# Optimization experiments

Hardware: AMD Instinct MI355X
Metric: run time of the kernel (lower is better)

Reference implementation:

```python
import jax, jax.numpy as jnp
import numpy as np

N_NODES = 10000
N_EDGES = 25000
D_FEAT = 128

def setup_inputs() -> dict:
    key = jax.random.key(0)
    k1, k2, k3 = jax.random.split(key, 3)
    x = jax.random.normal(k1, (N_NODES, D_FEAT), dtype=jnp.float32)
    edge_attr = jax.random.normal(k2, (N_EDGES, D_FEAT), dtype=jnp.float32)
    edge_index = jax.random.randint(k3, (2, N_EDGES), 0, N_NODES, dtype=jnp.int64)
    return {"x": x, "edge_attr": edge_attr, "edge_index": edge_index}

def reference(x, edge_attr, edge_index):
    # lg_node_idx: [E, 2] (src, dst) pairs; each original edge becomes a line-graph node
    lg_node_idx = edge_index.T
    # gather endpoint features and average -> [E, d]
    new_x = x[lg_node_idx].mean(axis=1)
    # stack([x, edge_attr], dim=2).mean(dim=2) == elementwise average
    new_x = (new_x + edge_attr) * 0.5
    col0 = lg_node_idx[:, 0]  # src of each edge
    col1 = lg_node_idx[:, 1]  # dst of each edge
    # edge i -> edge j connected iff dst(i) == src(j) and src(i) != dst(j)
    mask = (col1[:, None] == col0[None, :]) & (col0[:, None] != col1[None, :])  # [E, E]
    rows, cols = jnp.nonzero(mask)  # data-dependent size; eager (non-jit) reference
    lg_edge_index = jnp.stack([rows, cols], axis=0)  # [2, E_lg]
    # attr of line-graph edge = feature of shared node's incoming edge's dst entry
    lg_edge_attr_idx = lg_node_idx[rows][:, 1]
    lg_edge_attr = new_x[lg_edge_attr_idx]
    return new_x, lg_edge_index, lg_edge_attr
```

## Files before the change

### kernel.cpp

```cpp
#include <hip/hip_runtime.h>

#define NN 10000
#define NE 25000
#define DF 128
#define SB 256
#define NBLK ((NE + SB - 1) / SB)
#define NEWXB ((NE * 32 + SB - 1) / SB)

__global__ void k_init(int* __restrict__ head, int* __restrict__ gFlag) {
    int tid = blockIdx.x * blockDim.x + threadIdx.x;
    if (tid < NN) head[tid] = -1;
    if (tid < NBLK) gFlag[tid] = 0;
}

__global__ void k_link(const int* __restrict__ c0,
                       int* __restrict__ head, int* __restrict__ nxt) {
    int j = blockIdx.x * blockDim.x + threadIdx.x;
    if (j >= NE) return;
    nxt[j] = atomicExch(&head[c0[j]], j);
}

__global__ __launch_bounds__(SB) void k_scan_newx(const float* __restrict__ x,
                                                  const float* __restrict__ ea,
                                                  const int* __restrict__ c0,
                                                  const int* __restrict__ c1,
                                                  const int* __restrict__ head,
                                                  const int* __restrict__ nxt,
                                                  int* __restrict__ gFlag,
                                                  int* __restrict__ rowStart,
                                                  float* __restrict__ out) {
    int b = blockIdx.x, t = threadIdx.x;

    if (b >= NBLK) {
        int tid = (b - NBLK) * SB + t;
        if (tid >= NE * 32) return;
        int e = tid >> 5, q = tid & 31;
        int u = c0[e], v = c1[e];
        float4 a  = ((const float4*)(x + (size_t)u * DF))[q];
        float4 bb = ((const float4*)(x + (size_t)v * DF))[q];
        float4 c  = ((const float4*)(ea + (size_t)e * DF))[q];
        float4 r;
        r.x = ((a.x + bb.x) * 0.5f + c.x) * 0.5f;
        r.y = ((a.y + bb.y) * 0.5f + c.y) * 0.5f;
        r.z = ((a.z + bb.z) * 0.5f + c.z) * 0.5f;
        r.w = ((a.w + bb.w) * 0.5f + c.w) * 0.5f;
        ((float4*)(out + (size_t)e * DF))[q] = r;
        return;
    }

    __shared__ int sc[SB];
    __shared__ int sr[SB];
    int i = b * SB + t;
    int cnt = 0;
    if (i < NE) {
        int u = c0[i], v = c1[i];
        for (int j = head[v]; j != -1; j = nxt[j])
            if (c1[j] != u) ++cnt;
    }
    sc[t] = cnt;
    __syncthreads();
    for (int off = 1; off < SB; off <<= 1) {
        int add = (t >= off) ? sc[t - off] : 0;
        __syncthreads();
        sc[t] += add;
        __syncthreads();
    }
    int blockSum = sc[SB - 1];
    if (t == 0) atomicExch(&gFlag[b], blockSum + 1);
    int val = 0;
    if (t < b) {
        int v2;
        do { v2 = atomicAdd(&gFlag[t], 0); } while (v2 == 0);
        val = v2 - 1;
    }
    sr[t] = val;
    __syncthreads();
    for (int off = SB / 2; off > 0; off >>= 1) {
        if (t < off) sr[t] += sr[t + off];
        __syncthreads();
    }
    int base = sr[0];
    if (i < NE) rowStart[i] = base + sc[t] - cnt;
    if (b == NBLK - 1 && t == 0) rowStart[NE] = base + blockSum;
}

__global__ void k_emit(const float* __restrict__ newx,
                       const int* __restrict__ c0, const int* __restrict__ c1,
                       const int* __restrict__ head, const int* __restrict__ nxt,
                       const int* __restrict__ rowStart,
                       float* __restrict__ outRows, float* __restrict__ outCols,
                       float* __restrict__ outAttr) {
    int gtid = blockIdx.x * blockDim.x + threadIdx.x;
    int i = gtid >> 6, lane = gtid & 63;
    if (i >= NE) return;
    int base = rowStart[i];
    int cnt  = rowStart[i + 1] - base;
    if (cnt == 0) return;
    int u = c0[i], v = c1[i];

    int myj = -1, B = 0;
    for (int j = head[v]; j != -1; j = nxt[j], ++B)
        if (B == lane) myj = j;

    if (B <= 64) {
        int myc1 = (myj >= 0) ? c1[myj] : -1;
        bool keep = (myj >= 0) && (myc1 != u);
        int rank = 0;
        for (int q = 0; q < B; ++q) {
            int jq = __shfl(myj, q);
            int cq = __shfl(myc1, q);
            if (cq != u && jq < myj) ++rank;
        }
        if (keep) {
            outRows[base + rank] = (float)i;
            outCols[base + rank] = (float)myj;
        }
    } else {
        int pos = 0;
        for (int j = head[v]; j != -1; j = nxt[j], ++pos) {
            if ((pos & 63) != lane) continue;
            if (c1[j] == u) continue;
            int rank = 0;
            for (int j2 = head[v]; j2 != -1; j2 = nxt[j2])
                rank += (c1[j2] != u && j2 < j) ? 1 : 0;
            outRows[base + rank] = (float)i;
            outCols[base + rank] = (float)j;
        }
    }

    float4 val = ((const float4*)(newx + (size_t)v * DF))[lane & 31];
    for (int tt = (lane >> 5); tt < cnt; tt += 2)
        ((float4*)(outAttr + (size_t)(base + tt) * DF))[lane & 31] = val;
}


extern "C" void kernel_launch(void* const* d_in, const int* in_sizes, int n_in,
                              void* d_out, int out_size, void* d_ws, size_t ws_size,
                              hipStream_t stream) {
    const float* x  = (const float*)d_in[0];
    const float* ea = (const float*)d_in[1];
    const int*   ei = (const int*)d_in[2];
    const int* c0 = ei;
    const int* c1 = ei + NE;

    float* out = (float*)d_out;
    int E_lg = (out_size - NE * DF) / (DF + 2);
    if (E_lg < 0) E_lg = 0;

    float* out_newx = out;
    float* out_rows = out + (size_t)NE * DF;
    float* out_cols = out_rows + E_lg;
    float* out_attr = out_cols + E_lg;

    int* ws       = (int*)d_ws;
    int* head     = ws;
    int* nxt      = head + NN;
    int* rowStart = nxt + NE;
    int* gFlag    = rowStart + NE + 1;

    k_init<<<(NN + SB - 1) / SB, SB, 0, stream>>>(head, gFlag);
    k_link<<<(NE + SB - 1) / SB, SB, 0, stream>>>(c0, head, nxt);
    k_scan_newx<<<NBLK + NEWXB, SB, 0, stream>>>(x, ea, c0, c1, head, nxt,
                                                 gFlag, rowStart, out_newx);
    k_emit<<<(NE * 64 + SB - 1) / SB, SB, 0, stream>>>(out_newx, c0, c1, head, nxt,
                                                       rowStart, out_rows, out_cols, out_attr);
}
```

Baseline: 40.34 us.

## Move newx into init kernel and emit indices inside scan kernel

Measured after the change: 47.15 us. 1.17x slower.

```diff
diff --git a/kernel.cpp b/kernel.cpp
--- a/kernel.cpp
+++ b/kernel.cpp
@@ -7,10 +7,27 @@
 #define NBLK ((NE + SB - 1) / SB)
 #define NEWXB ((NE * 32 + SB - 1) / SB)
 
-__global__ void k_init(int* __restrict__ head, int* __restrict__ gFlag) {
+typedef float f4 __attribute__((ext_vector_type(4)));
+
+__global__ void k_newx_init(const float* __restrict__ x, const float* __restrict__ ea,
+                            const int* __restrict__ c0, const int* __restrict__ c1,
+                            float* __restrict__ out, int* __restrict__ head,
+                            int* __restrict__ gFlag) {
     int tid = blockIdx.x * blockDim.x + threadIdx.x;
     if (tid < NN) head[tid] = -1;
     if (tid < NBLK) gFlag[tid] = 0;
+    if (tid >= NE * 32) return;
+    int e = tid >> 5, q = tid & 31;
+    int u = c0[e], v = c1[e];
+    float4 a  = ((const float4*)(x + (size_t)u * DF))[q];
+    float4 bb = ((const float4*)(x + (size_t)v * DF))[q];
+    float4 c  = ((const float4*)(ea + (size_t)e * DF))[q];
+    float4 r;
+    r.x = ((a.x + bb.x) * 0.5f + c.x) * 0.5f;
+    r.y = ((a.y + bb.y) * 0.5f + c.y) * 0.5f;
+    r.z = ((a.z + bb.z) * 0.5f + c.z) * 0.5f;
+    r.w = ((a.w + bb.w) * 0.5f + c.w) * 0.5f;
+    ((float4*)(out + (size_t)e * DF))[q] = r;
 }
 
 __global__ void k_link(const int* __restrict__ c0,
@@ -20,40 +37,21 @@
     nxt[j] = atomicExch(&head[c0[j]], j);
 }
 
-__global__ __launch_bounds__(SB) void k_scan_newx(const float* __restrict__ x,
-                                                  const float* __restrict__ ea,
-                                                  const int* __restrict__ c0,
-                                                  const int* __restrict__ c1,
-                                                  const int* __restrict__ head,
-                                                  const int* __restrict__ nxt,
-                                                  int* __restrict__ gFlag,
-                                                  int* __restrict__ rowStart,
-                                                  float* __restrict__ out) {
-    int b = blockIdx.x, t = threadIdx.x;
-
-    if (b >= NBLK) {
-        int tid = (b - NBLK) * SB + t;
-        if (tid >= NE * 32) return;
-        int e = tid >> 5, q = tid & 31;
-        int u = c0[e], v = c1[e];
-        float4 a  = ((const float4*)(x + (size_t)u * DF))[q];
-        float4 bb = ((const float4*)(x + (size_t)v * DF))[q];
-        float4 c  = ((const float4*)(ea + (size_t)e * DF))[q];
-        float4 r;
-        r.x = ((a.x + bb.x) * 0.5f + c.x) * 0.5f;
-        r.y = ((a.y + bb.y) * 0.5f + c.y) * 0.5f;
-        r.z = ((a.z + bb.z) * 0.5f + c.z) * 0.5f;
-        r.w = ((a.w + bb.w) * 0.5f + c.w) * 0.5f;
-        ((float4*)(out + (size_t)e * DF))[q] = r;
-        return;
-    }
-
+__global__ __launch_bounds__(SB) void k_scan_idx(const int* __restrict__ c0,
+                                                 const int* __restrict__ c1,
+                                                 const int* __restrict__ head,
+                                                 const int* __restrict__ nxt,
+                                                 int* __restrict__ gFlag,
+                                                 float* __restrict__ outRows,
+                                                 float* __restrict__ outCols,
+                                                 int* __restrict__ attrSrc) {
     __shared__ int sc[SB];
     __shared__ int sr[SB];
+    int b = blockIdx.x, t = threadIdx.x;
     int i = b * SB + t;
-    int cnt = 0;
+    int u = 0, v = 0, cnt = 0;
     if (i < NE) {
-        int u = c0[i], v = c1[i];
+        u = c0[i]; v = c1[i];
         for (int j = head[v]; j != -1; j = nxt[j])
             if (c1[j] != u) ++cnt;
     }
@@ -79,58 +77,35 @@
         if (t < off) sr[t] += sr[t + off];
         __syncthreads();
     }
-    int base = sr[0];
-    if (i < NE) rowStart[i] = base + sc[t] - cnt;
-    if (b == NBLK - 1 && t == 0) rowStart[NE] = base + blockSum;
-}
+    int base = sr[0] + sc[t] - cnt;
 
-__global__ void k_emit(const float* __restrict__ newx,
-                       const int* __restrict__ c0, const int* __restrict__ c1,
-                       const int* __restrict__ head, const int* __restrict__ nxt,
-                       const int* __restrict__ rowStart,
-                       float* __restrict__ outRows, float* __restrict__ outCols,
-                       float* __restrict__ outAttr) {
-    int gtid = blockIdx.x * blockDim.x + threadIdx.x;
-    int i = gtid >> 6, lane = gtid & 63;
-    if (i >= NE) return;
-    int base = rowStart[i];
-    int cnt  = rowStart[i + 1] - base;
-    if (cnt == 0) return;
-    int u = c0[i], v = c1[i];
-
-    int myj = -1, B = 0;
-    for (int j = head[v]; j != -1; j = nxt[j], ++B)
-        if (B == lane) myj = j;
-
-    if (B <= 64) {
-        int myc1 = (myj >= 0) ? c1[myj] : -1;
-        bool keep = (myj >= 0) && (myc1 != u);
-        int rank = 0;
-        for (int q = 0; q < B; ++q) {
-            int jq = __shfl(myj, q);
-            int cq = __shfl(myc1, q);
-            if (cq != u && jq < myj) ++rank;
+    if (i < NE && cnt > 0) {
+        float fi = (float)i;
+        for (int t2 = 0; t2 < cnt; ++t2) {
+            __builtin_nontemporal_store(fi, &outRows[base + t2]);
+            attrSrc[base + t2] = v;
         }
-        if (keep) {
-            outRows[base + rank] = (float)i;
-            outCols[base + rank] = (float)myj;
-        }
-    } else {
-        int pos = 0;
-        for (int j = head[v]; j != -1; j = nxt[j], ++pos) {
-            if ((pos & 63) != lane) continue;
+        for (int j = head[v]; j != -1; j = nxt[j]) {
             if (c1[j] == u) continue;
             int rank = 0;
             for (int j2 = head[v]; j2 != -1; j2 = nxt[j2])
                 rank += (c1[j2] != u && j2 < j) ? 1 : 0;
-            outRows[base + rank] = (float)i;
-            outCols[base + rank] = (float)j;
+            __builtin_nontemporal_store((float)j, &outCols[base + rank]);
         }
     }
+}
 
-    float4 val = ((const float4*)(newx + (size_t)v * DF))[lane & 31];
-    for (int tt = (lane >> 5); tt < cnt; tt += 2)
-        ((float4*)(outAttr + (size_t)(base + tt) * DF))[lane & 31] = val;
+__global__ void k_gather(const float* __restrict__ newx,
+                         const int* __restrict__ attrSrc,
+                         float* __restrict__ outAttr, int elg) {
+    int gtid = blockIdx.x * blockDim.x + threadIdx.x;
+    int w = gtid >> 6, lane = gtid & 63;
+    int k = 2 * w + (lane >> 5);
+    if (k >= elg) return;
+    int src = attrSrc[k];
+    int q = lane & 31;
+    f4 val = ((const f4*)(newx + (size_t)src * DF))[q];
+    __builtin_nontemporal_store(val, &((f4*)(outAttr + (size_t)k * DF))[q]);
 }
 
 
@@ -152,16 +127,19 @@
     float* out_cols = out_rows + E_lg;
     float* out_attr = out_cols + E_lg;
 
-    int* ws       = (int*)d_ws;
-    int* head     = ws;
-    int* nxt      = head + NN;
-    int* rowStart = nxt + NE;
-    int* gFlag    = rowStart + NE + 1;
+    int* ws      = (int*)d_ws;
+    int* head    = ws;
+    int* nxt     = head + NN;
+    int* gFlag   = nxt + NE;
+    int* attrSrc = gFlag + NBLK;
 
-    k_init<<<(NN + SB - 1) / SB, SB, 0, stream>>>(head, gFlag);
+    k_newx_init<<<NEWXB, SB, 0, stream>>>(x, ea, c0, c1, out_newx, head, gFlag);
     k_link<<<(NE + SB - 1) / SB, SB, 0, stream>>>(c0, head, nxt);
-    k_scan_newx<<<NBLK + NEWXB, SB, 0, stream>>>(x, ea, c0, c1, head, nxt,
-                                                 gFlag, rowStart, out_newx);
-    k_emit<<<(NE * 64 + SB - 1) / SB, SB, 0, stream>>>(out_newx, c0, c1, head, nxt,
-                                                       rowStart, out_rows, out_cols, out_attr);
+    k_scan_idx<<<NBLK, SB, 0, stream>>>(c0, c1, head, nxt, gFlag,
+                                        out_rows, out_cols, attrSrc);
+    if (E_lg > 0) {
+        int waves = (E_lg + 1) / 2;
+        int blocks = (waves * 64 + SB - 1) / SB;
+        k_gather<<<blocks, SB, 0, stream>>>(out_newx, attrSrc, out_attr, E_lg);
+    }
 }
```
